# Optimization experiments

Measured on AMD Instinct MI355X. Metric: run time of the kernel, lower is better.

The kernel has to match this reference:

```python
import jax, jax.numpy as jnp
import numpy as np

D_MODEL = 256
D_STATE = 16
D_CONV = 4
EXPAND = 2
D_INNER = EXPAND * D_MODEL          # 512
DT_RANK = (D_MODEL + 15) // 16      # 16
B_SZ = 4
L_SEQ = 2048
EPS = 1e-5


def setup_inputs() -> dict:
    key = jax.random.key(0)
    ks = jax.random.split(key, 10)
    s = 0.02
    return {
        "x": jax.random.normal(ks[0], (B_SZ, L_SEQ, D_MODEL), jnp.float32),
        # Mamba params
        "in_proj_w": jax.random.normal(ks[1], (2 * D_INNER, D_MODEL), jnp.float32) * s,
        "conv_w": jax.random.normal(ks[2], (D_INNER, 1, D_CONV), jnp.float32) * s,  # depthwise
        "conv_b": jnp.zeros((D_INNER,), jnp.float32),
        "x_proj_w": jax.random.normal(ks[3], (DT_RANK + 2 * D_STATE, D_INNER), jnp.float32) * s,
        "dt_proj_w": jax.random.normal(ks[4], (D_INNER, DT_RANK), jnp.float32) * s,
        "dt_proj_b": jax.random.uniform(ks[5], (D_INNER,), jnp.float32, -4.0, -2.0),
        "A_log": jnp.log(jnp.broadcast_to(jnp.arange(1, D_STATE + 1, dtype=jnp.float32), (D_INNER, D_STATE))),
        "Dp": jnp.ones((D_INNER,), jnp.float32),
        "out_proj_w": jax.random.normal(ks[6], (D_MODEL, D_INNER), jnp.float32) * s,
        # LayerNorms
        "ln1_g": jnp.ones((D_MODEL,), jnp.float32), "ln1_b": jnp.zeros((D_MODEL,), jnp.float32),
        "ln2_g": jnp.ones((D_MODEL,), jnp.float32), "ln2_b": jnp.zeros((D_MODEL,), jnp.float32),
        # temp_enhance: Conv1d(d_model, d_model, k=3, pad=1, groups=4) + BatchNorm1d (eval buffers)
        "enh_w": jax.random.normal(ks[7], (D_MODEL, D_MODEL // 4, 3), jnp.float32) * s,
        "enh_b": jnp.zeros((D_MODEL,), jnp.float32),
        "bn_g": jnp.ones((D_MODEL,), jnp.float32), "bn_b": jnp.zeros((D_MODEL,), jnp.float32),
        "bn_mean": jnp.zeros((D_MODEL,), jnp.float32), "bn_var": jnp.ones((D_MODEL,), jnp.float32),
    }


def _layernorm(x, g, b):
    m = x.mean(-1, keepdims=True)
    v = ((x - m) ** 2).mean(-1, keepdims=True)
    return (x - m) * jax.lax.rsqrt(v + EPS) * g + b


def _mamba(x, in_proj_w, conv_w, conv_b, x_proj_w, dt_proj_w, dt_proj_b, A_log, Dp, out_proj_w):
    Bb, L, _ = x.shape
    # input projection -> gate z and conv stream
    xz = x @ in_proj_w.T                       # [B, L, 2*d_inner]
    xin, z = jnp.split(xz, 2, axis=-1)
    # causal depthwise conv over time
    xc = jnp.transpose(xin, (0, 2, 1))         # [B, d_inner, L]
    xc = jax.lax.conv_general_dilated(
        xc, conv_w, (1,), [(D_CONV - 1, 0)],
        dimension_numbers=("NCH", "OIH", "NCH"), feature_group_count=D_INNER)
    xc = xc + conv_b[None, :, None]
    xin = jax.nn.silu(jnp.transpose(xc, (0, 2, 1)))   # [B, L, d_inner]
    # input-dependent dt, B, C
    x_dbl = xin @ x_proj_w.T                   # [B, L, dt_rank + 2*d_state]
    dt, Bm, Cm = jnp.split(x_dbl, [DT_RANK, DT_RANK + D_STATE], axis=-1)
    dt = jax.nn.softplus(dt @ dt_proj_w.T + dt_proj_b)   # [B, L, d_inner]
    A = -jnp.exp(A_log)                         # [d_inner, d_state]
    dA = jnp.exp(dt[..., None] * A)             # [B, L, d_inner, d_state]
    dBx = dt[..., None] * Bm[:, :, None, :] * xin[..., None]
    # selective scan: h_t = dA_t * h_{t-1} + dBx_t ; y_t = <h_t, C_t>
    def step(h, inputs):
        a, bx, c = inputs
        h = a * h + bx                          # [B, d_inner, d_state]
        y = jnp.einsum("bds,bs->bd", h, c)
        return h, y
    h0 = jnp.zeros((Bb, D_INNER, D_STATE), x.dtype)
    _, ys = jax.lax.scan(step, h0, (jnp.transpose(dA, (1, 0, 2, 3)),
                                    jnp.transpose(dBx, (1, 0, 2, 3)),
                                    jnp.transpose(Cm, (1, 0, 2))))
    y = jnp.transpose(ys, (1, 0, 2)) + xin * Dp    # skip term D*x
    y = y * jax.nn.silu(z)
    return y @ out_proj_w.T


def reference(x, in_proj_w, conv_w, conv_b, x_proj_w, dt_proj_w, dt_proj_b, A_log, Dp,
              out_proj_w, ln1_g, ln1_b, ln2_g, ln2_b, enh_w, enh_b, bn_g, bn_b, bn_mean, bn_var):
    # dropout is identity in eval mode; BatchNorm uses running stats (eval)
    y = _mamba(x, in_proj_w, conv_w, conv_b, x_proj_w, dt_proj_w, dt_proj_b, A_log, Dp, out_proj_w)
    x1 = _layernorm(y, ln1_g, ln1_b)
    x2 = _layernorm(x + x1, ln2_g, ln2_b)
    # temp_enhance: grouped conv (groups=4) + BN(eval) + GELU on [B, C, L]
    xc = jnp.transpose(x2, (0, 2, 1))
    xc = jax.lax.conv_general_dilated(
        xc, enh_w, (1,), [(1, 1)],
        dimension_numbers=("NCH", "OIH", "NCH"), feature_group_count=4)
    xc = xc + enh_b[None, :, None]
    xc = (xc - bn_mean[None, :, None]) * jax.lax.rsqrt(bn_var[None, :, None] + EPS)
    xc = xc * bn_g[None, :, None] + bn_b[None, :, None]
    xc = jax.nn.gelu(xc, approximate=False)
    return x2 + jnp.transpose(xc, (0, 2, 1))
```

## Files before the change

### kernel.cpp

```cpp
#include <hip/hip_runtime.h>
#include <hip/hip_bf16.h>
#include <math.h>


typedef __attribute__((ext_vector_type(8))) short short8;
typedef __attribute__((ext_vector_type(4))) float f32x4;
typedef unsigned short ushortT;

#define NB    4
#define LSEQ  2048
#define DMODEL 256
#define DINNER 512
#define NTOK  8192
#define NCHUNK 128
#define CT    16
#define CTC   32
#define ET    16

__global__ __launch_bounds__(256) void k_prep(
    const float* __restrict__ x, const float* __restrict__ w_in,
    const float* __restrict__ w_out, const float* __restrict__ A_log,
    const float* __restrict__ xproj_w, const float* __restrict__ enh_w,
    const float* __restrict__ dtproj_w,
    __hip_bfloat16* __restrict__ xbf, __hip_bfloat16* __restrict__ wibf,
    __hip_bfloat16* __restrict__ wobf, float* __restrict__ A2L,
    __hip_bfloat16* __restrict__ xpbf, __hip_bfloat16* __restrict__ wenh,
    __hip_bfloat16* __restrict__ dtwp) {
  int i = blockIdx.x * 256 + threadIdx.x;
  if (i < NTOK * DMODEL)   xbf[i]  = __float2bfloat16(x[i]);
  if (i < 1024 * DMODEL)   wibf[i] = __float2bfloat16(w_in[i]);
  if (i < DMODEL * DINNER) wobf[i] = __float2bfloat16(w_out[i]);
  if (i < DINNER * 16)     A2L[i]  = -__expf(A_log[i]) * 1.44269504089f;
  if (i < 64 * 512) {
    int row = i >> 9, col = i & 511;
    xpbf[i] = __float2bfloat16(row < 48 ? xproj_w[row * 512 + col] : 0.0f);
  }
  if (i < 256 * 192) {
    int co = i / 192, k = i - co * 192;
    int kk = k >> 6, ci = k & 63;
    wenh[i] = __float2bfloat16(enh_w[co * 192 + ci * 3 + kk]);
  }
  if (i < 512 * 32) {
    int row = i >> 5, col = i & 31;
    dtwp[i] = __float2bfloat16(col < 16 ? dtproj_w[row * 16 + col] : 0.0f);
  }
}

__global__ __launch_bounds__(256) void gemm_bf(
    const ushortT* __restrict__ A, const ushortT* __restrict__ W,
    __hip_bfloat16* __restrict__ C, int M, int N, int K) {
  __shared__ __align__(16) ushortT Al[64 * 72];
  __shared__ __align__(16) ushortT Wl[64 * 72];
  int tid  = threadIdx.x;
  int mBase = blockIdx.x * 64, nBase = blockIdx.y * 64;
  int wv = tid >> 6, lane = tid & 63, lo = lane & 15, quad = lane >> 4;
  f32x4 acc[4] = {};
  for (int kt = 0; kt < K; kt += 64) {
#pragma unroll
    for (int q = 0; q < 2; ++q) {
      int cid = tid + q * 256;
      int r = cid >> 3, kc = (cid & 7) * 8;
      *(short8*)&Al[r * 72 + kc] = *(const short8*)&A[(size_t)(mBase + r) * K + kt + kc];
      *(short8*)&Wl[r * 72 + kc] = *(const short8*)&W[(size_t)(nBase + r) * K + kt + kc];
    }
    __syncthreads();
#pragma unroll
    for (int k0 = 0; k0 < 64; k0 += 32) {
      short8 bfrag = *(short8*)&Wl[(wv * 16 + lo) * 72 + k0 + quad * 8];
#pragma unroll
      for (int mb = 0; mb < 4; ++mb) {
        short8 afrag = *(short8*)&Al[(mb * 16 + lo) * 72 + k0 + quad * 8];
        acc[mb] = __builtin_amdgcn_mfma_f32_16x16x32_bf16(afrag, bfrag, acc[mb], 0, 0, 0);
      }
    }
    __syncthreads();
  }
#pragma unroll
  for (int mb = 0; mb < 4; ++mb)
#pragma unroll
    for (int r = 0; r < 4; ++r) {
      int row = mBase + mb * 16 + quad * 4 + r;
      int col = nBase + wv * 16 + lo;
      C[(size_t)row * N + col] = __float2bfloat16(acc[mb][r]);
    }
}

__device__ __forceinline__ float softplus_fast(float v) {
  return fmaxf(v, 0.0f) + __logf(1.0f + __expf(-fabsf(v)));
}

__global__ __launch_bounds__(512) void k_convproj(
    const __hip_bfloat16* __restrict__ xzbf, const float* __restrict__ conv_w,
    const float* __restrict__ conv_b, const ushortT* __restrict__ xpbf,
    const ushortT* __restrict__ dtwp, const float* __restrict__ dtb_,
    __hip_bfloat16* __restrict__ xcbf, float* __restrict__ xd,
    float* __restrict__ dtv_out) {
  __shared__ __align__(16) ushortT xct[CTC * 520];
  __shared__ __align__(16) ushortT xdt[32 * 32];
  int d = threadIdx.x;
  int t0 = blockIdx.x * CTC, b = blockIdx.y;
  const __hip_bfloat16* base = xzbf + (size_t)b * LSEQ * 1024 + d;
  float4 w4 = *(const float4*)&conv_w[d * 4];
  float cb = conv_b[d];
  float xm3 = 0.f, xm2 = 0.f, xm1 = 0.f;
  if (t0 > 0) {
    xm3 = __bfloat162float(base[(size_t)(t0 - 3) * 1024]);
    xm2 = __bfloat162float(base[(size_t)(t0 - 2) * 1024]);
    xm1 = __bfloat162float(base[(size_t)(t0 - 1) * 1024]);
  }
  size_t orow = (size_t)(b * LSEQ + t0) * 512 + d;
#pragma unroll 4
  for (int i = 0; i < CTC; ++i) {
    float xt = __bfloat162float(base[(size_t)(t0 + i) * 1024]);
    float acc = cb + w4.x * xm3 + w4.y * xm2 + w4.z * xm1 + w4.w * xt;
    float s = acc / (1.0f + __expf(-acc));
    __hip_bfloat16 sb = __float2bfloat16(s);
    xcbf[orow] = sb;
    xct[i * 520 + d] = *(ushortT*)&sb;
    orow += 512;
    xm3 = xm2; xm2 = xm1; xm1 = xt;
  }
  ((unsigned int*)xdt)[d] = 0u;
  __syncthreads();
  int wv = d >> 6, lane = d & 63, lo = lane & 15, quad = lane >> 4;
  int mt = wv & 1, nt = wv >> 1;
  f32x4 acc = {};
#pragma unroll
  for (int k0 = 0; k0 < 512; k0 += 32) {
    short8 af = *(short8*)&xct[(mt * 16 + lo) * 520 + k0 + quad * 8];
    short8 bf = *(const short8*)&xpbf[(size_t)(nt * 16 + lo) * 512 + k0 + quad * 8];
    acc = __builtin_amdgcn_mfma_f32_16x16x32_bf16(af, bf, acc, 0, 0, 0);
  }
  int tokb = b * LSEQ + t0;
#pragma unroll
  for (int r = 0; r < 4; ++r)
    xd[(size_t)(tokb + mt * 16 + quad * 4 + r) * 64 + nt * 16 + lo] = acc[r];
  if (wv < 2) {
#pragma unroll
    for (int r = 0; r < 4; ++r) {
      __hip_bfloat16 hb = __float2bfloat16(acc[r]);
      xdt[(mt * 16 + quad * 4 + r) * 32 + lo] = *(ushortT*)&hb;
    }
  }
  __syncthreads();
  int mt2 = wv & 1, ntb = (wv >> 1) * 8;
  short8 af2 = *(short8*)&xdt[(mt2 * 16 + lo) * 32 + quad * 8];
#pragma unroll
  for (int i = 0; i < 8; ++i) {
    int ntc = ntb + i;
    short8 bf2 = *(const short8*)&dtwp[(size_t)(ntc * 16 + lo) * 32 + quad * 8];
    f32x4 a2 = __builtin_amdgcn_mfma_f32_16x16x32_bf16(af2, bf2, (f32x4){}, 0, 0, 0);
    int dd = ntc * 16 + lo;
    float bias = dtb_[dd];
#pragma unroll
    for (int r = 0; r < 4; ++r) {
      float dtv = softplus_fast(a2[r] + bias);
      dtv_out[(size_t)(tokb + mt2 * 16 + quad * 4 + r) * 512 + dd] = dtv;
    }
  }
}

__device__ __forceinline__ void decay_powers(float a1, float* aa) {
  aa[0] = a1;
#pragma unroll
  for (int s = 1; s < 16; ++s) aa[s] = aa[(s - 1) >> 1] * aa[s >> 1];
}

__global__ __launch_bounds__(512) void k_scanA(
    const __hip_bfloat16* __restrict__ xcbf, const float* __restrict__ xd,
    const float* __restrict__ dtvbuf, const float* __restrict__ A2L,
    float* __restrict__ Sd, float* __restrict__ Hend) {
  int tid = threadIdx.x;
  int c = blockIdx.x, b = blockIdx.y;
  int tok0 = b * LSEQ + c * CT;
  int d = tid;
  float a2l0 = A2L[d * 16];
  float h[16];
#pragma unroll
  for (int s = 0; s < 16; ++s) h[s] = 0.0f;
  float sdt = 0.0f;
  for (int t = 0; t < CT; ++t) {
    const float4* Bp = (const float4*)&xd[(size_t)(tok0 + t) * 64 + 16];
    float4 B0 = Bp[0], B1 = Bp[1], B2 = Bp[2], B3 = Bp[3];
    float dtv = dtvbuf[(size_t)(tok0 + t) * 512 + d];
    sdt += dtv;
    float xv = __bfloat162float(xcbf[(size_t)(tok0 + t) * 512 + d]);
    float ux = dtv * xv;
    float aa[16];
    decay_powers(exp2f(dtv * a2l0), aa);
    float Bv[16] = {B0.x, B0.y, B0.z, B0.w, B1.x, B1.y, B1.z, B1.w,
                    B2.x, B2.y, B2.z, B2.w, B3.x, B3.y, B3.z, B3.w};
#pragma unroll
    for (int s = 0; s < 16; ++s)
      h[s] = aa[s] * h[s] + ux * Bv[s];
  }
  Sd[(size_t)(b * NCHUNK + c) * 512 + d] = sdt;
  size_t basei = ((size_t)(b * NCHUNK + c) * 512 + d) * 16;
#pragma unroll
  for (int q = 0; q < 4; ++q)
    *(float4*)&Hend[basei + q * 4] = make_float4(h[q*4], h[q*4+1], h[q*4+2], h[q*4+3]);
}

__global__ __launch_bounds__(256) void k_scanB(
    const float* __restrict__ Sd, float* __restrict__ Hend,
    const float* __restrict__ A2L) {
  int gid = blockIdx.x * 256 + threadIdx.x;
  int b = gid >> 13, rem = gid & 8191, d = rem >> 4;
  float a2lv = A2L[rem];
  float carry = 0.f;
  for (int c = 0; c < NCHUNK; ++c) {
    float sdt = Sd[(size_t)(b * NCHUNK + c) * 512 + d];
    size_t idx = (size_t)(b * NCHUNK + c) * 8192 + rem;
    float p  = exp2f(a2lv * sdt);
    float he = Hend[idx];
    Hend[idx] = carry;
    carry = p * carry + he;
  }
}

__global__ __launch_bounds__(512) void k_scanC(
    const __hip_bfloat16* __restrict__ xcbf, const float* __restrict__ xd,
    const float* __restrict__ dtvbuf, const float* __restrict__ A2L,
    const float* __restrict__ Hinit, const __hip_bfloat16* __restrict__ xzbf,
    const float* __restrict__ Dp, const ushortT* __restrict__ wobf,
    float* __restrict__ y2) {
  __shared__ __align__(16) ushortT yt[CT * 520];
  int tid = threadIdx.x;
  int c = blockIdx.x, b = blockIdx.y;
  int tok0 = b * LSEQ + c * CT;
  int d = tid;
  float a2l0 = A2L[d * 16];
  float h[16];
  size_t basei = ((size_t)(b * NCHUNK + c) * 512 + d) * 16;
#pragma unroll
  for (int q = 0; q < 4; ++q) {
    float4 hv = *(const float4*)&Hinit[basei + q * 4];
    h[q*4] = hv.x; h[q*4+1] = hv.y; h[q*4+2] = hv.z; h[q*4+3] = hv.w;
  }
  float dpv = Dp[d];
  for (int t = 0; t < CT; ++t) {
    const float4* Bp = (const float4*)&xd[(size_t)(tok0 + t) * 64 + 16];
    float4 B0 = Bp[0], B1 = Bp[1], B2 = Bp[2], B3 = Bp[3];
    float4 C0 = Bp[4], C1 = Bp[5], C2 = Bp[6], C3 = Bp[7];
    float dtv = dtvbuf[(size_t)(tok0 + t) * 512 + d];
    float xv = __bfloat162float(xcbf[(size_t)(tok0 + t) * 512 + d]);
    float zv = __bfloat162float(xzbf[(size_t)(tok0 + t) * 1024 + 512 + d]);
    float ux = dtv * xv;
    float aa[16];
    decay_powers(exp2f(dtv * a2l0), aa);
    float Bv[16] = {B0.x, B0.y, B0.z, B0.w, B1.x, B1.y, B1.z, B1.w,
                    B2.x, B2.y, B2.z, B2.w, B3.x, B3.y, B3.z, B3.w};
    float Cv[16] = {C0.x, C0.y, C0.z, C0.w, C1.x, C1.y, C1.z, C1.w,
                    C2.x, C2.y, C2.z, C2.w, C3.x, C3.y, C3.z, C3.w};
    float y = 0.f;
#pragma unroll
    for (int s = 0; s < 16; ++s) {
      h[s] = aa[s] * h[s] + ux * Bv[s];
      y += h[s] * Cv[s];
    }
    y = (y + xv * dpv) * (zv / (1.0f + __expf(-zv)));
    __hip_bfloat16 yb = __float2bfloat16(y);
    yt[t * 520 + d] = *(ushortT*)&yb;
  }
  __syncthreads();
  int wv = tid >> 6, lane = tid & 63, lo = lane & 15, quad = lane >> 4;
  f32x4 a0 = {}, a1 = {};
#pragma unroll
  for (int k0 = 0; k0 < 512; k0 += 32) {
    short8 af = *(short8*)&yt[lo * 520 + k0 + quad * 8];
    short8 b0 = *(const short8*)&wobf[(size_t)(wv * 32 + lo) * 512 + k0 + quad * 8];
    short8 b1 = *(const short8*)&wobf[(size_t)(wv * 32 + 16 + lo) * 512 + k0 + quad * 8];
    a0 = __builtin_amdgcn_mfma_f32_16x16x32_bf16(af, b0, a0, 0, 0, 0);
    a1 = __builtin_amdgcn_mfma_f32_16x16x32_bf16(af, b1, a1, 0, 0, 0);
  }
#pragma unroll
  for (int r = 0; r < 4; ++r) {
    int row = tok0 + quad * 4 + r;
    y2[(size_t)row * 256 + wv * 32 + lo]      = a0[r];
    y2[(size_t)row * 256 + wv * 32 + 16 + lo] = a1[r];
  }
}

__global__ __launch_bounds__(256) void k_lnenh(
    const float* __restrict__ y2, const float* __restrict__ x,
    const float* __restrict__ g1, const float* __restrict__ b1,
    const float* __restrict__ g2, const float* __restrict__ b2,
    const ushortT* __restrict__ wenh, const float* __restrict__ enh_b,
    const float* __restrict__ bn_g, const float* __restrict__ bn_b,
    const float* __restrict__ bn_mean, const float* __restrict__ bn_var,
    float* __restrict__ out) {
  __shared__ __align__(16) float   x2f[18 * 264];
  __shared__ __align__(16) ushortT x2h[18 * 264];
  int tid = threadIdx.x, wv = tid >> 6, lane = tid & 63;
  int tb = blockIdx.x, b = blockIdx.y;
  int tbase = tb * ET;
  for (int r = wv; r < 18; r += 4) {
    int t = tbase - 1 + r;
    float4 o = make_float4(0.f, 0.f, 0.f, 0.f);
    if (t >= 0 && t < LSEQ) {
      int tok = b * LSEQ + t;
      float4 v = ((const float4*)&y2[(size_t)tok * DMODEL])[lane];
      float s = v.x + v.y + v.z + v.w;
#pragma unroll
      for (int off = 32; off; off >>= 1) s += __shfl_xor(s, off);
      float m = s * (1.0f / DMODEL);
      float4 dv = make_float4(v.x - m, v.y - m, v.z - m, v.w - m);
      float q = dv.x*dv.x + dv.y*dv.y + dv.z*dv.z + dv.w*dv.w;
#pragma unroll
      for (int off = 32; off; off >>= 1) q += __shfl_xor(q, off);
      float rs = rsqrtf(q * (1.0f / DMODEL) + 1e-5f);
      float4 gg = ((const float4*)g1)[lane], bb = ((const float4*)b1)[lane];
      float4 xv = ((const float4*)&x[(size_t)tok * DMODEL])[lane];
      float4 tt;
      tt.x = xv.x + dv.x * rs * gg.x + bb.x;
      tt.y = xv.y + dv.y * rs * gg.y + bb.y;
      tt.z = xv.z + dv.z * rs * gg.z + bb.z;
      tt.w = xv.w + dv.w * rs * gg.w + bb.w;
      float s2 = tt.x + tt.y + tt.z + tt.w;
#pragma unroll
      for (int off = 32; off; off >>= 1) s2 += __shfl_xor(s2, off);
      float m2 = s2 * (1.0f / DMODEL);
      float4 d2 = make_float4(tt.x - m2, tt.y - m2, tt.z - m2, tt.w - m2);
      float q2 = d2.x*d2.x + d2.y*d2.y + d2.z*d2.z + d2.w*d2.w;
#pragma unroll
      for (int off = 32; off; off >>= 1) q2 += __shfl_xor(q2, off);
      float rs2 = rsqrtf(q2 * (1.0f / DMODEL) + 1e-5f);
      float4 g2v = ((const float4*)g2)[lane], b2v = ((const float4*)b2)[lane];
      o.x = d2.x * rs2 * g2v.x + b2v.x;
      o.y = d2.y * rs2 * g2v.y + b2v.y;
      o.z = d2.z * rs2 * g2v.z + b2v.z;
      o.w = d2.w * rs2 * g2v.w + b2v.w;
    }
    *(float4*)&x2f[r * 264 + lane * 4] = o;
    ushortT p[4];
    __hip_bfloat16 hb;
    hb = __float2bfloat16(o.x); p[0] = *(ushortT*)&hb;
    hb = __float2bfloat16(o.y); p[1] = *(ushortT*)&hb;
    hb = __float2bfloat16(o.z); p[2] = *(ushortT*)&hb;
    hb = __float2bfloat16(o.w); p[3] = *(ushortT*)&hb;
    *(uint2*)&x2h[r * 264 + lane * 4] = *(uint2*)p;
  }
  __syncthreads();
  int g = wv, lo = lane & 15, quad = lane >> 4;
  short8 af[6];
#pragma unroll
  for (int ks = 0; ks < 6; ++ks) {
    int kk = ks >> 1, cb = (ks & 1) * 32;
    af[ks] = *(short8*)&x2h[(lo + kk) * 264 + g * 64 + cb + quad * 8];
  }
  f32x4 acc[4] = {};
#pragma unroll
  for (int nt = 0; nt < 4; ++nt) {
    int co = g * 64 + nt * 16 + lo;
#pragma unroll
    for (int ks = 0; ks < 6; ++ks) {
      short8 bf = *(const short8*)&wenh[(size_t)co * 192 + ks * 32 + quad * 8];
      acc[nt] = __builtin_amdgcn_mfma_f32_16x16x32_bf16(af[ks], bf, acc[nt], 0, 0, 0);
    }
  }
#pragma unroll
  for (int nt = 0; nt < 4; ++nt) {
    int co = g * 64 + nt * 16 + lo;
    float scale = bn_g[co] * rsqrtf(bn_var[co] + 1e-5f);
    float shift = bn_b[co] - bn_mean[co] * scale;
    float ebv = enh_b[co];
#pragma unroll
    for (int r = 0; r < 4; ++r) {
      int m = quad * 4 + r;
      float v = (acc[nt][r] + ebv) * scale + shift;
      float ge = 0.5f * v * (1.0f + erff(v * 0.70710678118f));
      out[(size_t)(b * LSEQ + tbase + m) * DMODEL + co] = x2f[(m + 1) * 264 + co] + ge;
    }
  }
}

extern "C" void kernel_launch(void* const* d_in, const int* in_sizes, int n_in,
                              void* d_out, int out_size, void* d_ws, size_t ws_size,
                              hipStream_t stream) {
  const float* x        = (const float*)d_in[0];
  const float* in_w     = (const float*)d_in[1];
  const float* conv_w   = (const float*)d_in[2];
  const float* conv_b   = (const float*)d_in[3];
  const float* xproj_w  = (const float*)d_in[4];
  const float* dtproj_w = (const float*)d_in[5];
  const float* dtproj_b = (const float*)d_in[6];
  const float* A_log    = (const float*)d_in[7];
  const float* Dp       = (const float*)d_in[8];
  const float* out_w    = (const float*)d_in[9];
  const float* ln1_g    = (const float*)d_in[10];
  const float* ln1_b    = (const float*)d_in[11];
  const float* ln2_g    = (const float*)d_in[12];
  const float* ln2_b    = (const float*)d_in[13];
  const float* enh_w    = (const float*)d_in[14];
  const float* enh_b    = (const float*)d_in[15];
  const float* bn_g     = (const float*)d_in[16];
  const float* bn_b     = (const float*)d_in[17];
  const float* bn_mean  = (const float*)d_in[18];
  const float* bn_var   = (const float*)d_in[19];
  float* out = (float*)d_out;

  char* ws = (char*)d_ws;
  size_t off = 0;
  auto alloc = [&](size_t bytes) { char* p = ws + off; off += (bytes + 255) & ~(size_t)255; return p; };
  __hip_bfloat16* xzbf = (__hip_bfloat16*)alloc((size_t)NTOK * 1024 * 2);
  __hip_bfloat16* xcbf = (__hip_bfloat16*)alloc((size_t)NTOK * 512 * 2);
  float*          xd   = (float*)alloc((size_t)NTOK * 64 * 4);
  float*          dtv  = (float*)alloc((size_t)NTOK * 512 * 4);
  float*          A2L  = (float*)alloc((size_t)DINNER * 16 * 4);
  __hip_bfloat16* xbf  = (__hip_bfloat16*)alloc((size_t)NTOK * DMODEL * 2);
  __hip_bfloat16* wibf = (__hip_bfloat16*)alloc((size_t)1024 * DMODEL * 2);
  __hip_bfloat16* wobf = (__hip_bfloat16*)alloc((size_t)DMODEL * DINNER * 2);
  __hip_bfloat16* xpbf = (__hip_bfloat16*)alloc((size_t)64 * 512 * 2);
  __hip_bfloat16* wenh = (__hip_bfloat16*)alloc((size_t)256 * 192 * 2);
  __hip_bfloat16* dtwp = (__hip_bfloat16*)alloc((size_t)512 * 32 * 2);
  float*          Sd   = (float*)alloc((size_t)NB * NCHUNK * 512 * 4);
  float*          He   = (float*)alloc((size_t)NB * NCHUNK * 512 * 16 * 4);
  float*          y2   = (float*)alloc((size_t)NTOK * DMODEL * 4);
  (void)ws_size; (void)in_sizes; (void)n_in; (void)out_size;

  k_prep<<<8192, 256, 0, stream>>>(x, in_w, out_w, A_log, xproj_w, enh_w, dtproj_w,
                                   xbf, wibf, wobf, A2L, xpbf, wenh, dtwp);
  gemm_bf<<<dim3(128, 16), 256, 0, stream>>>((const ushortT*)xbf, (const ushortT*)wibf,
                                             xzbf, NTOK, 1024, DMODEL);
  k_convproj<<<dim3(64, 4), 512, 0, stream>>>(xzbf, conv_w, conv_b,
                                              (const ushortT*)xpbf, (const ushortT*)dtwp,
                                              dtproj_b, xcbf, xd, dtv);
  k_scanA<<<dim3(NCHUNK, 4), 512, 0, stream>>>(xcbf, xd, dtv, A2L, Sd, He);
  k_scanB<<<128, 256, 0, stream>>>(Sd, He, A2L);
  k_scanC<<<dim3(NCHUNK, 4), 512, 0, stream>>>(xcbf, xd, dtv, A2L, He, xzbf, Dp,
                                               (const ushortT*)wobf, y2);
  k_lnenh<<<dim3(LSEQ / ET, 4), 256, 0, stream>>>(y2, x, ln1_g, ln1_b, ln2_g, ln2_b,
                                                  (const ushortT*)wenh, enh_b,
                                                  bn_g, bn_b, bn_mean, bn_var, out);
}
```

Baseline: 204.5 us.

## Fuse conv/projection with chunk scan and convert x to bf16 inside GEMM

```diff
diff --git a/kernel.cpp b/kernel.cpp
--- a/kernel.cpp
+++ b/kernel.cpp
@@ -17,17 +17,19 @@
 #define CTC   32
 #define ET    16
 
+__device__ __forceinline__ ushortT bf16bits(float f) {
+  __hip_bfloat16 h = __float2bfloat16(f);
+  return *(ushortT*)&h;
+}
+
 __global__ __launch_bounds__(256) void k_prep(
-    const float* __restrict__ x, const float* __restrict__ w_in,
-    const float* __restrict__ w_out, const float* __restrict__ A_log,
-    const float* __restrict__ xproj_w, const float* __restrict__ enh_w,
-    const float* __restrict__ dtproj_w,
-    __hip_bfloat16* __restrict__ xbf, __hip_bfloat16* __restrict__ wibf,
-    __hip_bfloat16* __restrict__ wobf, float* __restrict__ A2L,
-    __hip_bfloat16* __restrict__ xpbf, __hip_bfloat16* __restrict__ wenh,
-    __hip_bfloat16* __restrict__ dtwp) {
+    const float* __restrict__ w_in, const float* __restrict__ w_out,
+    const float* __restrict__ A_log, const float* __restrict__ xproj_w,
+    const float* __restrict__ enh_w, const float* __restrict__ dtproj_w,
+    __hip_bfloat16* __restrict__ wibf, __hip_bfloat16* __restrict__ wobf,
+    float* __restrict__ A2L, __hip_bfloat16* __restrict__ xpbf,
+    __hip_bfloat16* __restrict__ wenh, __hip_bfloat16* __restrict__ dtwp) {
   int i = blockIdx.x * 256 + threadIdx.x;
-  if (i < NTOK * DMODEL)   xbf[i]  = __float2bfloat16(x[i]);
   if (i < 1024 * DMODEL)   wibf[i] = __float2bfloat16(w_in[i]);
   if (i < DMODEL * DINNER) wobf[i] = __float2bfloat16(w_out[i]);
   if (i < DINNER * 16)     A2L[i]  = -__expf(A_log[i]) * 1.44269504089f;
@@ -47,7 +49,7 @@
 }
 
 __global__ __launch_bounds__(256) void gemm_bf(
-    const ushortT* __restrict__ A, const ushortT* __restrict__ W,
+    const float* __restrict__ A, const ushortT* __restrict__ W,
     __hip_bfloat16* __restrict__ C, int M, int N, int K) {
   __shared__ __align__(16) ushortT Al[64 * 72];
   __shared__ __align__(16) ushortT Wl[64 * 72];
@@ -60,7 +62,15 @@
     for (int q = 0; q < 2; ++q) {
       int cid = tid + q * 256;
       int r = cid >> 3, kc = (cid & 7) * 8;
-      *(short8*)&Al[r * 72 + kc] = *(const short8*)&A[(size_t)(mBase + r) * K + kt + kc];
+      const float* src = &A[(size_t)(mBase + r) * K + kt + kc];
+      float4 f0 = *(const float4*)src;
+      float4 f1 = *(const float4*)(src + 4);
+      short8 v;
+      v[0] = (short)bf16bits(f0.x); v[1] = (short)bf16bits(f0.y);
+      v[2] = (short)bf16bits(f0.z); v[3] = (short)bf16bits(f0.w);
+      v[4] = (short)bf16bits(f1.x); v[5] = (short)bf16bits(f1.y);
+      v[6] = (short)bf16bits(f1.z); v[7] = (short)bf16bits(f1.w);
+      *(short8*)&Al[r * 72 + kc] = v;
       *(short8*)&Wl[r * 72 + kc] = *(const short8*)&W[(size_t)(nBase + r) * K + kt + kc];
     }
     __syncthreads();
@@ -89,14 +99,25 @@
   return fmaxf(v, 0.0f) + __logf(1.0f + __expf(-fabsf(v)));
 }
 
-__global__ __launch_bounds__(512) void k_convproj(
+__device__ __forceinline__ void decay_powers(float a1, float* aa) {
+  aa[0] = a1;
+#pragma unroll
+  for (int s = 1; s < 16; ++s) aa[s] = aa[(s - 1) >> 1] * aa[s >> 1];
+}
+
+__global__ __launch_bounds__(512) void k_convscan(
     const __hip_bfloat16* __restrict__ xzbf, const float* __restrict__ conv_w,
     const float* __restrict__ conv_b, const ushortT* __restrict__ xpbf,
     const ushortT* __restrict__ dtwp, const float* __restrict__ dtb_,
+    const float* __restrict__ A2L,
     __hip_bfloat16* __restrict__ xcbf, float* __restrict__ xd,
-    float* __restrict__ dtv_out) {
-  __shared__ __align__(16) ushortT xct[CTC * 520];
+    float* __restrict__ dtv_out, float* __restrict__ Sd,
+    float* __restrict__ Hend) {
+  __shared__ __align__(16) char smem[CTC * 520 * 2];
+  ushortT* xct = (ushortT*)smem;
+  float*   dtt = (float*)smem;
   __shared__ __align__(16) ushortT xdt[32 * 32];
+  __shared__ __align__(16) float   Bt[CTC * 16];
   int d = threadIdx.x;
   int t0 = blockIdx.x * CTC, b = blockIdx.y;
   const __hip_bfloat16* base = xzbf + (size_t)b * LSEQ * 1024 + d;
@@ -108,8 +129,9 @@
     xm2 = __bfloat162float(base[(size_t)(t0 - 2) * 1024]);
     xm1 = __bfloat162float(base[(size_t)(t0 - 1) * 1024]);
   }
+  float xvr[CTC];
   size_t orow = (size_t)(b * LSEQ + t0) * 512 + d;
-#pragma unroll 4
+#pragma unroll
   for (int i = 0; i < CTC; ++i) {
     float xt = __bfloat162float(base[(size_t)(t0 + i) * 1024]);
     float acc = cb + w4.x * xm3 + w4.y * xm2 + w4.z * xm1 + w4.w * xt;
@@ -117,6 +139,7 @@
     __hip_bfloat16 sb = __float2bfloat16(s);
     xcbf[orow] = sb;
     xct[i * 520 + d] = *(ushortT*)&sb;
+    xvr[i] = __bfloat162float(sb);
     orow += 512;
     xm3 = xm2; xm2 = xm1; xm1 = xt;
   }
@@ -135,16 +158,20 @@
 #pragma unroll
   for (int r = 0; r < 4; ++r)
     xd[(size_t)(tokb + mt * 16 + quad * 4 + r) * 64 + nt * 16 + lo] = acc[r];
-  if (wv < 2) {
-#pragma unroll
-    for (int r = 0; r < 4; ++r) {
-      __hip_bfloat16 hb = __float2bfloat16(acc[r]);
-      xdt[(mt * 16 + quad * 4 + r) * 32 + lo] = *(ushortT*)&hb;
-    }
+  if (nt == 0) {
+#pragma unroll
+    for (int r = 0; r < 4; ++r)
+      xdt[(mt * 16 + quad * 4 + r) * 32 + lo] = bf16bits(acc[r]);
+  }
+  if (nt == 1) {
+#pragma unroll
+    for (int r = 0; r < 4; ++r)
+      Bt[(mt * 16 + quad * 4 + r) * 16 + lo] = acc[r];
   }
   __syncthreads();
   int mt2 = wv & 1, ntb = (wv >> 1) * 8;
   short8 af2 = *(short8*)&xdt[(mt2 * 16 + lo) * 32 + quad * 8];
+  float dtvr[32];
 #pragma unroll
   for (int i = 0; i < 8; ++i) {
     int ntc = ntb + i;
@@ -155,50 +182,53 @@
 #pragma unroll
     for (int r = 0; r < 4; ++r) {
       float dtv = softplus_fast(a2[r] + bias);
+      dtvr[i * 4 + r] = dtv;
       dtv_out[(size_t)(tokb + mt2 * 16 + quad * 4 + r) * 512 + dd] = dtv;
     }
   }
-}
-
-__device__ __forceinline__ void decay_powers(float a1, float* aa) {
-  aa[0] = a1;
-#pragma unroll
-  for (int s = 1; s < 16; ++s) aa[s] = aa[(s - 1) >> 1] * aa[s >> 1];
-}
-
-__global__ __launch_bounds__(512) void k_scanA(
-    const __hip_bfloat16* __restrict__ xcbf, const float* __restrict__ xd,
-    const float* __restrict__ dtvbuf, const float* __restrict__ A2L,
-    float* __restrict__ Sd, float* __restrict__ Hend) {
-  int tid = threadIdx.x;
-  int c = blockIdx.x, b = blockIdx.y;
-  int tok0 = b * LSEQ + c * CT;
-  int d = tid;
   float a2l0 = A2L[d * 16];
-  float h[16];
-#pragma unroll
-  for (int s = 0; s < 16; ++s) h[s] = 0.0f;
-  float sdt = 0.0f;
-  for (int t = 0; t < CT; ++t) {
-    const float4* Bp = (const float4*)&xd[(size_t)(tok0 + t) * 64 + 16];
-    float4 B0 = Bp[0], B1 = Bp[1], B2 = Bp[2], B3 = Bp[3];
-    float dtv = dtvbuf[(size_t)(tok0 + t) * 512 + d];
-    sdt += dtv;
-    float xv = __bfloat162float(xcbf[(size_t)(tok0 + t) * 512 + d]);
-    float ux = dtv * xv;
-    float aa[16];
-    decay_powers(exp2f(dtv * a2l0), aa);
-    float Bv[16] = {B0.x, B0.y, B0.z, B0.w, B1.x, B1.y, B1.z, B1.w,
-                    B2.x, B2.y, B2.z, B2.w, B3.x, B3.y, B3.z, B3.w};
-#pragma unroll
-    for (int s = 0; s < 16; ++s)
-      h[s] = aa[s] * h[s] + ux * Bv[s];
-  }
-  Sd[(size_t)(b * NCHUNK + c) * 512 + d] = sdt;
-  size_t basei = ((size_t)(b * NCHUNK + c) * 512 + d) * 16;
-#pragma unroll
-  for (int q = 0; q < 4; ++q)
-    *(float4*)&Hend[basei + q * 4] = make_float4(h[q*4], h[q*4+1], h[q*4+2], h[q*4+3]);
+#pragma unroll
+  for (int cc = 0; cc < 2; ++cc) {
+    __syncthreads();
+    if (mt2 == cc) {
+#pragma unroll
+      for (int i = 0; i < 8; ++i) {
+        int dd = (ntb + i) * 16 + lo;
+#pragma unroll
+        for (int r = 0; r < 4; ++r)
+          dtt[(quad * 4 + r) * 512 + dd] = dtvr[i * 4 + r];
+      }
+    }
+    __syncthreads();
+    float h[16];
+#pragma unroll
+    for (int s = 0; s < 16; ++s) h[s] = 0.0f;
+    float sdt = 0.0f;
+#pragma unroll
+    for (int t = 0; t < CT; ++t) {
+      int tt = cc * CT + t;
+      float dtv = dtt[t * 512 + d];
+      float xv = xvr[tt];
+      const float4* Bp = (const float4*)&Bt[tt * 16];
+      float4 B0 = Bp[0], B1 = Bp[1], B2 = Bp[2], B3 = Bp[3];
+      sdt += dtv;
+      float ux = dtv * xv;
+      float aa[16];
+      decay_powers(exp2f(dtv * a2l0), aa);
+      float Bv[16] = {B0.x, B0.y, B0.z, B0.w, B1.x, B1.y, B1.z, B1.w,
+                      B2.x, B2.y, B2.z, B2.w, B3.x, B3.y, B3.z, B3.w};
+#pragma unroll
+      for (int s = 0; s < 16; ++s)
+        h[s] = aa[s] * h[s] + ux * Bv[s];
+    }
+    int c = blockIdx.x * 2 + cc;
+    Sd[(size_t)(b * NCHUNK + c) * 512 + d] = sdt;
+    size_t basei = ((size_t)(b * NCHUNK + c) * 512 + d) * 16;
+#pragma unroll
+    for (int q = 0; q < 4; ++q)
+      *(float4*)&Hend[basei + q * 4] =
+          make_float4(h[q * 4], h[q * 4 + 1], h[q * 4 + 2], h[q * 4 + 3]);
+  }
 }
 
 __global__ __launch_bounds__(256) void k_scanB(
@@ -207,14 +237,25 @@
   int gid = blockIdx.x * 256 + threadIdx.x;
   int b = gid >> 13, rem = gid & 8191, d = rem >> 4;
   float a2lv = A2L[rem];
+  const float* SdB = &Sd[(size_t)b * NCHUNK * 512 + d];
+  float* HeB = &Hend[(size_t)b * NCHUNK * 8192 + rem];
   float carry = 0.f;
-  for (int c = 0; c < NCHUNK; ++c) {
-    float sdt = Sd[(size_t)(b * NCHUNK + c) * 512 + d];
-    size_t idx = (size_t)(b * NCHUNK + c) * 8192 + rem;
-    float p  = exp2f(a2lv * sdt);
-    float he = Hend[idx];
-    Hend[idx] = carry;
-    carry = p * carry + he;
+#pragma unroll 1
+  for (int c = 0; c < NCHUNK; c += 4) {
+    float s0 = SdB[(size_t)(c + 0) * 512];
+    float s1 = SdB[(size_t)(c + 1) * 512];
+    float s2 = SdB[(size_t)(c + 2) * 512];
+    float s3 = SdB[(size_t)(c + 3) * 512];
+    float h0 = HeB[(size_t)(c + 0) * 8192];
+    float h1 = HeB[(size_t)(c + 1) * 8192];
+    float h2 = HeB[(size_t)(c + 2) * 8192];
+    float h3 = HeB[(size_t)(c + 3) * 8192];
+    float p0 = exp2f(a2lv * s0), p1 = exp2f(a2lv * s1);
+    float p2 = exp2f(a2lv * s2), p3 = exp2f(a2lv * s3);
+    HeB[(size_t)(c + 0) * 8192] = carry; carry = p0 * carry + h0;
+    HeB[(size_t)(c + 1) * 8192] = carry; carry = p1 * carry + h1;
+    HeB[(size_t)(c + 2) * 8192] = carry; carry = p2 * carry + h2;
+    HeB[(size_t)(c + 3) * 8192] = carry; carry = p3 * carry + h3;
   }
 }
 
@@ -333,11 +374,8 @@
     }
     *(float4*)&x2f[r * 264 + lane * 4] = o;
     ushortT p[4];
-    __hip_bfloat16 hb;
-    hb = __float2bfloat16(o.x); p[0] = *(ushortT*)&hb;
-    hb = __float2bfloat16(o.y); p[1] = *(ushortT*)&hb;
-    hb = __float2bfloat16(o.z); p[2] = *(ushortT*)&hb;
-    hb = __float2bfloat16(o.w); p[3] = *(ushortT*)&hb;
+    p[0] = bf16bits(o.x); p[1] = bf16bits(o.y);
+    p[2] = bf16bits(o.z); p[3] = bf16bits(o.w);
     *(uint2*)&x2h[r * 264 + lane * 4] = *(uint2*)p;
   }
   __syncthreads();
@@ -407,7 +445,6 @@
   float*          xd   = (float*)alloc((size_t)NTOK * 64 * 4);
   float*          dtv  = (float*)alloc((size_t)NTOK * 512 * 4);
   float*          A2L  = (float*)alloc((size_t)DINNER * 16 * 4);
-  __hip_bfloat16* xbf  = (__hip_bfloat16*)alloc((size_t)NTOK * DMODEL * 2);
   __hip_bfloat16* wibf = (__hip_bfloat16*)alloc((size_t)1024 * DMODEL * 2);
   __hip_bfloat16* wobf = (__hip_bfloat16*)alloc((size_t)DMODEL * DINNER * 2);
   __hip_bfloat16* xpbf = (__hip_bfloat16*)alloc((size_t)64 * 512 * 2);
@@ -418,14 +455,13 @@
   float*          y2   = (float*)alloc((size_t)NTOK * DMODEL * 4);
   (void)ws_size; (void)in_sizes; (void)n_in; (void)out_size;
 
-  k_prep<<<8192, 256, 0, stream>>>(x, in_w, out_w, A_log, xproj_w, enh_w, dtproj_w,
-                                   xbf, wibf, wobf, A2L, xpbf, wenh, dtwp);
-  gemm_bf<<<dim3(128, 16), 256, 0, stream>>>((const ushortT*)xbf, (const ushortT*)wibf,
+  k_prep<<<1024, 256, 0, stream>>>(in_w, out_w, A_log, xproj_w, enh_w, dtproj_w,
+                                   wibf, wobf, A2L, xpbf, wenh, dtwp);
+  gemm_bf<<<dim3(128, 16), 256, 0, stream>>>(x, (const ushortT*)wibf,
                                              xzbf, NTOK, 1024, DMODEL);
-  k_convproj<<<dim3(64, 4), 512, 0, stream>>>(xzbf, conv_w, conv_b,
+  k_convscan<<<dim3(64, 4), 512, 0, stream>>>(xzbf, conv_w, conv_b,
                                               (const ushortT*)xpbf, (const ushortT*)dtwp,
-                                              dtproj_b, xcbf, xd, dtv);
-  k_scanA<<<dim3(NCHUNK, 4), 512, 0, stream>>>(xcbf, xd, dtv, A2L, Sd, He);
+                                              dtproj_b, A2L, xcbf, xd, dtv, Sd, He);
   k_scanB<<<128, 256, 0, stream>>>(Sd, He, A2L);
   k_scanC<<<dim3(NCHUNK, 4), 512, 0, stream>>>(xcbf, xd, dtv, A2L, He, xzbf, Dp,
                                                (const ushortT*)wobf, y2);
```

After: 199.0 us. 1.03x faster.
